# Performance work log

Measured on AMD Instinct MI355X. Metric: run time of the kernel, lower is better.

The kernel has to match this reference:

```python
import jax, jax.numpy as jnp
import numpy as np

N = 100000
E = 1600000
BN_EPS = 1e-3  # Keras BatchNormalization default epsilon


def setup_inputs() -> dict:
    key = jax.random.key(0)
    ks = jax.random.split(key, 24)
    inp = {
        'x': jax.random.normal(ks[0], (N, 128), jnp.float32),
        'edge_src': jax.random.randint(ks[1], (E,), 0, N, jnp.int32),
        'edge_dst': jnp.sort(jax.random.randint(ks[2], (E,), 0, N, jnp.int32)),
        'edge_w': jax.random.uniform(ks[3], (E,), jnp.float32),
        'bn1_gamma': jnp.ones((128,), jnp.float32),
        'bn1_beta': jnp.zeros((128,), jnp.float32),
        'bn1_mean': jax.random.normal(ks[4], (128,), jnp.float32),
        'bn1_var': jax.random.uniform(ks[5], (128,), jnp.float32),
        'gat_w': jax.random.normal(ks[6], (128, 128), jnp.float32) * 0.09,
        'gat_a_self': jax.random.normal(ks[7], (128,), jnp.float32) * 0.09,
        'gat_a_nbr': jax.random.normal(ks[8], (128,), jnp.float32) * 0.09,
        'gat_b': jnp.zeros((128,), jnp.float32),
        'bn2_gamma': jnp.ones((128,), jnp.float32),
        'bn2_beta': jnp.zeros((128,), jnp.float32),
        'bn2_mean': jax.random.normal(ks[9], (128,), jnp.float32),
        'bn2_var': jax.random.uniform(ks[10], (128,), jnp.float32),
        'gcn2_w': jax.random.normal(ks[11], (128, 64), jnp.float32) * 0.09,
        'gcn2_b': jnp.zeros((64,), jnp.float32),
        'bn3_gamma': jnp.ones((64,), jnp.float32),
        'bn3_beta': jnp.zeros((64,), jnp.float32),
        'bn3_mean': jax.random.normal(ks[12], (64,), jnp.float32),
        'bn3_var': jax.random.uniform(ks[13], (64,), jnp.float32),
        'gcn3_w': jax.random.normal(ks[14], (64, 32), jnp.float32) * 0.12,
        'gcn3_b': jnp.zeros((32,), jnp.float32),
        'zm_w': jax.random.normal(ks[15], (32, 64), jnp.float32) * 0.18,
        'zm_b': jnp.zeros((64,), jnp.float32),
        'zv_w': jax.random.normal(ks[16], (32, 64), jnp.float32) * 0.18,
        'zv_b': jnp.zeros((64,), jnp.float32),
        'eps': jax.random.normal(ks[17], (N, 64), jnp.float32),
    }
    return inp


def _bn(x, gamma, beta, mean, var):
    # Keras BatchNormalization, inference mode (moving statistics).
    return gamma * (x - mean) * jax.lax.rsqrt(var + BN_EPS) + beta


def _gat(x, edge_src, edge_dst, w, a_self, a_nbr, b, n):
    h = x @ w                                   # [N, C]
    att_i = h @ a_self                          # [N] target score
    att_j = h @ a_nbr                           # [N] source score
    e = jax.nn.leaky_relu(att_i[edge_dst] + att_j[edge_src], 0.2)  # [E]
    m = jax.ops.segment_max(e, edge_dst, num_segments=n)
    p = jnp.exp(e - m[edge_dst])
    s = jax.ops.segment_sum(p, edge_dst, num_segments=n)
    alpha = p / s[edge_dst]                     # segment softmax over in-edges
    out = jax.ops.segment_sum(alpha[:, None] * h[edge_src], edge_dst, num_segments=n)
    return jax.nn.relu(out + b)


def _gcn(x, edge_src, edge_dst, edge_w, w, b, n):
    h = x @ w                                   # [N, C]
    out = jax.ops.segment_sum(edge_w[:, None] * h[edge_src], edge_dst, num_segments=n)
    return jax.nn.relu(out + b)


def reference(x, edge_src, edge_dst, edge_w,
              bn1_gamma, bn1_beta, bn1_mean, bn1_var,
              gat_w, gat_a_self, gat_a_nbr, gat_b,
              bn2_gamma, bn2_beta, bn2_mean, bn2_var,
              gcn2_w, gcn2_b,
              bn3_gamma, bn3_beta, bn3_mean, bn3_var,
              gcn3_w, gcn3_b,
              zm_w, zm_b, zv_w, zv_b, eps):
    n = x.shape[0]
    h = _bn(x, bn1_gamma, bn1_beta, bn1_mean, bn1_var)
    h = _gat(h, edge_src, edge_dst, gat_w, gat_a_self, gat_a_nbr, gat_b, n)
    # dropout layers are identity at inference
    h = _bn(h, bn2_gamma, bn2_beta, bn2_mean, bn2_var)
    h = _gcn(h, edge_src, edge_dst, edge_w, gcn2_w, gcn2_b, n)
    h = _bn(h, bn3_gamma, bn3_beta, bn3_mean, bn3_var)
    h = _gcn(h, edge_src, edge_dst, edge_w, gcn3_w, gcn3_b, n)
    # Flatten on [N, F] is identity
    z_mean = jax.nn.sigmoid(h @ zm_w + zm_b)
    z_log_var = h @ zv_w + zv_b
    z = z_mean + jnp.exp(0.5 * z_log_var) * eps
    return (z_mean, z_log_var, z)
```

## Files before the change

kernel.cpp:

```cpp
#include <hip/hip_runtime.h>
#include <math.h>


#define BN_EPS 1e-3f

typedef __attribute__((ext_vector_type(8))) short bf16x8;
typedef __attribute__((ext_vector_type(4))) float f32x4;
typedef __attribute__((ext_vector_type(2))) float f32x2;

__device__ __forceinline__ f32x2 pkfma(f32x2 a, f32x2 b, f32x2 c) {
  f32x2 d;
  asm("v_pk_fma_f32 %0, %1, %2, %3" : "=v"(d) : "v"(a), "v"(b), "v"(c));
  return d;
}

__device__ __forceinline__ unsigned bf2(float lo, float hi) {
  unsigned ul = __float_as_uint(lo), uh = __float_as_uint(hi);
  ul = (ul + 0x7FFFu + ((ul >> 16) & 1u)) >> 16;
  uh = (uh + 0x7FFFu + ((uh >> 16) & 1u)) >> 16;
  return ul | (uh << 16);
}
__device__ __forceinline__ unsigned short bf1(float x) {
  unsigned u = __float_as_uint(x);
  return (unsigned short)((u + 0x7FFFu + ((u >> 16) & 1u)) >> 16);
}
__device__ __forceinline__ f32x2 ub2(unsigned u) {
  f32x2 r;
  r.x = __uint_as_float(u << 16);
  r.y = __uint_as_float(u & 0xFFFF0000u);
  return r;
}

__global__ __launch_bounds__(256) void prep_rowptr_kernel(
    const float* __restrict__ bn1g, const float* __restrict__ bn1b,
    const float* __restrict__ bn1m, const float* __restrict__ bn1v,
    const float* __restrict__ gatw,
    const float* __restrict__ bn2g, const float* __restrict__ bn2b,
    const float* __restrict__ bn2m, const float* __restrict__ bn2v,
    const float* __restrict__ gcn2w,
    const float* __restrict__ bn3g, const float* __restrict__ bn3b,
    const float* __restrict__ bn3m, const float* __restrict__ bn3v,
    const float* __restrict__ gcn3w,
    unsigned short* __restrict__ Wt1b, float* __restrict__ bW1,
    unsigned short* __restrict__ Wt2b, float* __restrict__ bW2,
    unsigned short* __restrict__ Wt3b, float* __restrict__ bW3,
    const int* __restrict__ dst, int* __restrict__ rp, int n, int e) {
  const int t = threadIdx.x;
  if (blockIdx.x != 0) {
    int i = (blockIdx.x - 1) * 256 + t;
    if (i > n) return;
    int lo = 0, hi = e;
    while (lo < hi) {
      int mid = (lo + hi) >> 1;
      if (dst[mid] < i) lo = mid + 1; else hi = mid;
    }
    rp[i] = lo;
    return;
  }
  __shared__ float a1[128], b1[128], a2[128], b2[128], a3[64], b3[64];
  if (t < 128) {
    float a = bn1g[t] * (1.0f / sqrtf(bn1v[t] + BN_EPS));
    a1[t] = a; b1[t] = bn1b[t] - bn1m[t] * a;
    float c = bn2g[t] * (1.0f / sqrtf(bn2v[t] + BN_EPS));
    a2[t] = c; b2[t] = bn2b[t] - bn2m[t] * c;
    if (t < 64) {
      float d = bn3g[t] * (1.0f / sqrtf(bn3v[t] + BN_EPS));
      a3[t] = d; b3[t] = bn3b[t] - bn3m[t] * d;
    }
  }
  __syncthreads();
  for (int idx = t; idx < 128 * 128; idx += 256) {
    int c = idx >> 7, k = idx & 127;
    Wt1b[idx] = bf1(a1[k] * gatw[k * 128 + c]);
  }
  for (int idx = t; idx < 64 * 128; idx += 256) {
    int c = idx >> 7, k = idx & 127;
    Wt2b[idx] = bf1(a2[k] * gcn2w[k * 64 + c]);
  }
  for (int idx = t; idx < 32 * 64; idx += 256) {
    int c = idx >> 6, k = idx & 63;
    Wt3b[idx] = bf1(a3[k] * gcn3w[k * 32 + c]);
  }
  if (t < 128) { float s = 0.f; for (int k = 0; k < 128; k++) s += b1[k] * gatw[k * 128 + t]; bW1[t] = s; }
  if (t < 64)  { float s = 0.f; for (int k = 0; k < 128; k++) s += b2[k] * gcn2w[k * 64 + t]; bW2[t] = s; }
  if (t < 32)  { float s = 0.f; for (int k = 0; k < 64; k++)  s += b3[k] * gcn3w[k * 32 + t]; bW3[t] = s; }
}

template <int K, int C, bool DO_ATT, bool IN_BF16>
__global__ __launch_bounds__(256) void gemm_mfma(
    const void* __restrict__ in, const unsigned short* __restrict__ Wtb,
    const float* __restrict__ bW, unsigned short* __restrict__ outb, int n,
    const float* __restrict__ aself, const float* __restrict__ anbr,
    float* __restrict__ atti, float* __restrict__ attj) {
  constexpr int KCH = K / 32;
  constexpr int MB = C / 16;
  const int wid = (blockIdx.x << 2) + (threadIdx.x >> 6);
  const int lane = threadIdx.x & 63;
  const int node0 = wid * 16;
  if (node0 >= n) return;
  const int ln = lane & 15;
  const int kg = lane >> 4;
  const int nd = node0 + ln;
  const int ndc = (nd < n) ? nd : (n - 1);
  bf16x8 bfr[KCH];
  if constexpr (IN_BF16) {
    const bf16x8* __restrict__ inr =
        (const bf16x8*)((const unsigned short*)in + (size_t)ndc * K);
#pragma unroll
    for (int kc = 0; kc < KCH; kc++) bfr[kc] = inr[kc * 4 + kg];
  } else {
    const float4* __restrict__ inr =
        (const float4*)((const float*)in + (size_t)ndc * K);
#pragma unroll
    for (int kc = 0; kc < KCH; kc++) {
      float4 u0 = inr[kc * 8 + kg * 2];
      float4 u1 = inr[kc * 8 + kg * 2 + 1];
      union { uint4 u; bf16x8 v; } pk;
      pk.u.x = bf2(u0.x, u0.y); pk.u.y = bf2(u0.z, u0.w);
      pk.u.z = bf2(u1.x, u1.y); pk.u.w = bf2(u1.z, u1.w);
      bfr[kc] = pk.v;
    }
  }
  float sa = 0.f, sj = 0.f;
#pragma unroll
  for (int m = 0; m < MB; m++) {
    f32x4 acc = {0.f, 0.f, 0.f, 0.f};
#pragma unroll
    for (int kc = 0; kc < KCH; kc++) {
      bf16x8 af = *(const bf16x8*)&Wtb[(size_t)(m * 16 + ln) * K + kc * 32 + kg * 8];
      acc = __builtin_amdgcn_mfma_f32_16x16x32_bf16(af, bfr[kc], acc, 0, 0, 0);
    }
    const int c0 = m * 16 + kg * 4;
    float4 bv = *(const float4*)&bW[c0];
    float o0 = acc[0] + bv.x, o1 = acc[1] + bv.y;
    float o2 = acc[2] + bv.z, o3 = acc[3] + bv.w;
    if (nd < n) {
      uint2 p; p.x = bf2(o0, o1); p.y = bf2(o2, o3);
      *(uint2*)&outb[(size_t)nd * C + c0] = p;
    }
    if constexpr (DO_ATT) {
      float4 as = *(const float4*)&aself[c0];
      float4 an = *(const float4*)&anbr[c0];
      sa += o0 * as.x + o1 * as.y + o2 * as.z + o3 * as.w;
      sj += o0 * an.x + o1 * an.y + o2 * an.z + o3 * an.w;
    }
  }
  if constexpr (DO_ATT) {
    sa += __shfl_xor(sa, 16); sa += __shfl_xor(sa, 32);
    sj += __shfl_xor(sj, 16); sj += __shfl_xor(sj, 32);
    if (kg == 0 && nd < n) { atti[nd] = sa; attj[nd] = sj; }
  }
}

__global__ __launch_bounds__(256) void gat_kernel(
    const unsigned short* __restrict__ h1b, const float* __restrict__ att_i,
    const float* __restrict__ att_j, const int* __restrict__ src,
    const int* __restrict__ rp, const float* __restrict__ bias,
    unsigned short* __restrict__ outb, int n) {
  const int node = (blockIdx.x * 256 + threadIdx.x) >> 5;
  const int sl = threadIdx.x & 31;
  const int gbase = threadIdx.x & 32;
  if (node >= n) return;
  const int start = rp[node];
  const int deg = rp[node + 1] - start;
  if (deg == 0) {
    float4 b = ((const float4*)bias)[sl];
    uint2 p;
    p.x = bf2(fmaxf(b.x, 0.f), fmaxf(b.y, 0.f));
    p.y = bf2(fmaxf(b.z, 0.f), fmaxf(b.w, 0.f));
    ((uint2*)outb)[(unsigned)node * 32 + sl] = p;
    return;
  }
  const uint2* __restrict__ h2v = (const uint2*)h1b;
  const float ai = att_i[node];
  f32x2 av[8];
#pragma unroll
  for (int k = 0; k < 8; k++) av[k] = {0.f, 0.f};
  float ss = 0.f, m_run = -INFINITY;
  for (int chunk = 0; chunk < deg; chunk += 32) {
    const int cnt = min(32, deg - chunk);
    int sv = 0; float v = -INFINITY;
    if (sl < cnt) {
      sv = src[start + chunk + sl];
      float a = ai + att_j[sv];
      v = (a >= 0.f) ? a : 0.2f * a;
    }
    float m = v;
#pragma unroll
    for (int off = 16; off; off >>= 1) m = fmaxf(m, __shfl_xor(m, off));
    const float m_new = fmaxf(m_run, m);
    if (chunk) {
      const float scale = __expf(m_run - m_new);
#pragma unroll
      for (int k = 0; k < 8; k++) { av[k].x *= scale; av[k].y *= scale; }
      ss *= scale;
    }
    const float p = (sl < cnt) ? __expf(v - m_new) : 0.f;
    float ps = p;
#pragma unroll
    for (int off = 16; off; off >>= 1) ps += __shfl_xor(ps, off);
    ss += ps;
    m_run = m_new;
    for (int j2 = 0; j2 < cnt; j2 += 8) {
      float pk[8]; int sk[8];
#pragma unroll
      for (int k = 0; k < 8; k++) {
        int j = gbase + j2 + k;
        pk[k] = __shfl(p, j);
        sk[k] = __shfl(sv, j);
      }
      uint2 hk[8];
#pragma unroll
      for (int k = 0; k < 8; k++) hk[k] = h2v[(unsigned)sk[k] * 32 + sl];
#pragma unroll
      for (int k = 0; k < 8; k++) {
        f32x2 pd = {pk[k], pk[k]};
        av[(k & 3) * 2]     = pkfma(ub2(hk[k].x), pd, av[(k & 3) * 2]);
        av[(k & 3) * 2 + 1] = pkfma(ub2(hk[k].y), pd, av[(k & 3) * 2 + 1]);
      }
    }
  }
  f32x2 s0, s1;
  s0.x = av[0].x + av[2].x + av[4].x + av[6].x;
  s0.y = av[0].y + av[2].y + av[4].y + av[6].y;
  s1.x = av[1].x + av[3].x + av[5].x + av[7].x;
  s1.y = av[1].y + av[3].y + av[5].y + av[7].y;
  const float inv = 1.0f / ss;
  float4 b = ((const float4*)bias)[sl];
  float o0 = fmaxf(fmaf(s0.x, inv, b.x), 0.f);
  float o1 = fmaxf(fmaf(s0.y, inv, b.y), 0.f);
  float o2 = fmaxf(fmaf(s1.x, inv, b.z), 0.f);
  float o3 = fmaxf(fmaf(s1.y, inv, b.w), 0.f);
  uint2 p; p.x = bf2(o0, o1); p.y = bf2(o2, o3);
  ((uint2*)outb)[(unsigned)node * 32 + sl] = p;
}

template <int C, int NCH>
__global__ __launch_bounds__(256) void gcn_agg_kernel(
    const unsigned short* __restrict__ hb, const int* __restrict__ src,
    const float* __restrict__ ew, const int* __restrict__ rp,
    const float* __restrict__ bias, unsigned short* __restrict__ outb, int n) {
  constexpr int CG = C / 4;
  constexpr int EGN = 64 / CG;
  const int node = (blockIdx.x * 256 + threadIdx.x) >> 6;
  const int lane = threadIdx.x & 63;
  if (node >= n) return;
  const int cg = lane % CG;
  const int eg = lane / CG;
  const int start = rp[node];
  const int deg = rp[node + 1] - start;
  const uint2* __restrict__ h2v = (const uint2*)hb;
  f32x2 av[8];
#pragma unroll
  for (int k = 0; k < 8; k++) av[k] = {0.f, 0.f};
  for (int chunk = 0; chunk < deg; chunk += 64) {
    const int cnt = min(64, deg - chunk);
    int sv = 0; float wv = 0.f;
    if (lane < cnt) {
      sv = src[start + chunk + lane];
      wv = ew[start + chunk + lane];
    }
    for (int j2 = 0; j2 < cnt; j2 += NCH * EGN) {
      float wk[NCH]; int sk[NCH];
#pragma unroll
      for (int k = 0; k < NCH; k++) {
        int j = j2 + k * EGN + eg;
        wk[k] = __shfl(wv, j);
        sk[k] = __shfl(sv, j);
      }
      uint2 hk[NCH];
#pragma unroll
      for (int k = 0; k < NCH; k++) hk[k] = h2v[(unsigned)sk[k] * CG + cg];
#pragma unroll
      for (int k = 0; k < NCH; k++) {
        f32x2 wd = {wk[k], wk[k]};
        av[(k & 3) * 2]     = pkfma(ub2(hk[k].x), wd, av[(k & 3) * 2]);
        av[(k & 3) * 2 + 1] = pkfma(ub2(hk[k].y), wd, av[(k & 3) * 2 + 1]);
      }
    }
  }
  float a0 = av[0].x + av[2].x + av[4].x + av[6].x;
  float a1 = av[0].y + av[2].y + av[4].y + av[6].y;
  float a2 = av[1].x + av[3].x + av[5].x + av[7].x;
  float a3 = av[1].y + av[3].y + av[5].y + av[7].y;
#pragma unroll
  for (int off = CG; off < 64; off <<= 1) {
    a0 += __shfl_xor(a0, off); a1 += __shfl_xor(a1, off);
    a2 += __shfl_xor(a2, off); a3 += __shfl_xor(a3, off);
  }
  if (eg == 0) {
    float4 b = ((const float4*)bias)[cg];
    float o0 = fmaxf(a0 + b.x, 0.f);
    float o1 = fmaxf(a1 + b.y, 0.f);
    float o2 = fmaxf(a2 + b.z, 0.f);
    float o3 = fmaxf(a3 + b.w, 0.f);
    uint2 p; p.x = bf2(o0, o1); p.y = bf2(o2, o3);
    ((uint2*)outb)[(unsigned)node * CG + cg] = p;
  }
}

__global__ __launch_bounds__(256) void final_kernel(
    const unsigned short* __restrict__ g3b, const float* __restrict__ zmw,
    const float* __restrict__ zmb, const float* __restrict__ zvw,
    const float* __restrict__ zvb, const float* __restrict__ eps,
    float* __restrict__ out, int n) {
  __shared__ float wm[32 * 64];
  __shared__ float wv[32 * 64];
  __shared__ float xs[4 * 32];
  for (int idx = threadIdx.x; idx < 2048; idx += 256) {
    wm[idx] = zmw[idx];
    wv[idx] = zvw[idx];
  }
  const float bm = zmb[threadIdx.x & 63];
  const float bv = zvb[threadIdx.x & 63];
  const size_t n64 = (size_t)n * 64;
  for (int pass = 0; pass < 16; pass++) {
    const int nb = blockIdx.x * 64 + pass * 4;
    __syncthreads();
    if (threadIdx.x < 128) {
      size_t idx = (size_t)nb * 32 + threadIdx.x;
      float vv = 0.f;
      if (idx < (size_t)n * 32)
        vv = __uint_as_float((unsigned)g3b[idx] << 16);
      xs[threadIdx.x] = vv;
    }
    __syncthreads();
    const int node = nb + (threadIdx.x >> 6);
    if (node >= n) continue;
    const int c = threadIdx.x & 63;
    const float* x = &xs[(threadIdx.x >> 6) * 32];
    float am = 0.f, avv = 0.f;
#pragma unroll
    for (int k = 0; k < 32; k++) {
      float xv = x[k];
      am = fmaf(xv, wm[k * 64 + c], am);
      avv = fmaf(xv, wv[k * 64 + c], avv);
    }
    am += bm;
    avv += bv;
    float zm = 1.f / (1.f + __expf(-am));
    float ex = __expf(fminf(0.5f * avv, 85.0f));
    float z = fmaf(ex, eps[(size_t)node * 64 + c], zm);
    size_t o = (size_t)node * 64 + c;
    out[o] = zm;
    out[n64 + o] = avv;
    out[2 * n64 + o] = z;
  }
}

extern "C" void kernel_launch(void* const* d_in, const int* in_sizes, int n_in,
                              void* d_out, int out_size, void* d_ws, size_t ws_size,
                              hipStream_t stream) {
  const float* x     = (const float*)d_in[0];
  const int*   esrc  = (const int*)d_in[1];
  const int*   edst  = (const int*)d_in[2];
  const float* ew    = (const float*)d_in[3];
  const float* bn1g  = (const float*)d_in[4];
  const float* bn1b  = (const float*)d_in[5];
  const float* bn1m  = (const float*)d_in[6];
  const float* bn1v  = (const float*)d_in[7];
  const float* gatw  = (const float*)d_in[8];
  const float* aself = (const float*)d_in[9];
  const float* anbr  = (const float*)d_in[10];
  const float* gatb  = (const float*)d_in[11];
  const float* bn2g  = (const float*)d_in[12];
  const float* bn2b  = (const float*)d_in[13];
  const float* bn2m  = (const float*)d_in[14];
  const float* bn2v  = (const float*)d_in[15];
  const float* gcn2w = (const float*)d_in[16];
  const float* gcn2b = (const float*)d_in[17];
  const float* bn3g  = (const float*)d_in[18];
  const float* bn3b  = (const float*)d_in[19];
  const float* bn3m  = (const float*)d_in[20];
  const float* bn3v  = (const float*)d_in[21];
  const float* gcn3w = (const float*)d_in[22];
  const float* gcn3b = (const float*)d_in[23];
  const float* zmw   = (const float*)d_in[24];
  const float* zmb   = (const float*)d_in[25];
  const float* zvw   = (const float*)d_in[26];
  const float* zvb   = (const float*)d_in[27];
  const float* eps   = (const float*)d_in[28];
  float* out = (float*)d_out;

  const int n = in_sizes[0] / 128;
  const int E = in_sizes[1];

  char* base = (char*)d_ws;
  size_t off = 0;
  auto alloc = [&](size_t bytes) -> char* {
    char* p = base + off;
    off += (bytes + 255) & ~(size_t)255;
    return p;
  };
  int*   rp   = (int*)alloc((size_t)(n + 1) * 4);
  unsigned short* Wt1b = (unsigned short*)alloc(128 * 128 * 2);
  float* bW1  = (float*)alloc(128 * 4);
  unsigned short* Wt2b = (unsigned short*)alloc(64 * 128 * 2);
  float* bW2  = (float*)alloc(64 * 4);
  unsigned short* Wt3b = (unsigned short*)alloc(32 * 64 * 2);
  float* bW3  = (float*)alloc(32 * 4);
  float* atti = (float*)alloc((size_t)n * 4);
  float* attj = (float*)alloc((size_t)n * 4);
  unsigned short* h1b = (unsigned short*)alloc((size_t)n * 128 * 2);
  unsigned short* g1b = (unsigned short*)alloc((size_t)n * 128 * 2);
  unsigned short* h2b = (unsigned short*)alloc((size_t)n * 64 * 2);
  unsigned short* g2b = h1b;
  unsigned short* h3b = g1b;
  unsigned short* g3b = h2b;

  const int rpb = (n + 1 + 255) / 256;
  prep_rowptr_kernel<<<rpb + 1, 256, 0, stream>>>(
      bn1g, bn1b, bn1m, bn1v, gatw, bn2g, bn2b, bn2m, bn2v, gcn2w,
      bn3g, bn3b, bn3m, bn3v, gcn3w,
      Wt1b, bW1, Wt2b, bW2, Wt3b, bW3, edst, rp, n, E);

  const int gw = (n + 15) / 16;
  const int gb = (gw + 3) / 4;

  gemm_mfma<128, 128, true, false><<<gb, 256, 0, stream>>>(
      x, Wt1b, bW1, h1b, n, aself, anbr, atti, attj);
  gat_kernel<<<(n + 7) / 8, 256, 0, stream>>>(
      h1b, atti, attj, esrc, rp, gatb, g1b, n);

  gemm_mfma<128, 64, false, true><<<gb, 256, 0, stream>>>(
      g1b, Wt2b, bW2, h2b, n, nullptr, nullptr, nullptr, nullptr);
  gcn_agg_kernel<64, 8><<<(n + 3) / 4, 256, 0, stream>>>(
      h2b, esrc, ew, rp, gcn2b, g2b, n);

  gemm_mfma<64, 32, false, true><<<gb, 256, 0, stream>>>(
      g2b, Wt3b, bW3, h3b, n, nullptr, nullptr, nullptr, nullptr);
  gcn_agg_kernel<32, 4><<<(n + 3) / 4, 256, 0, stream>>>(
      h3b, esrc, ew, rp, gcn3b, g3b, n);

  final_kernel<<<(n + 63) / 64, 256, 0, stream>>>(
      g3b, zmw, zmb, zvw, zvb, eps, out, n);
}
```

Baseline: 438.5 us.

## Map GCN aggregation to lane subgroups per node instead of whole wavefronts

The GCN aggregation kernel now gives each destination node a subgroup of C/4 lanes (16 or 8) instead of a full 64-lane wavefront. Several nodes therefore share one wavefront, and each subgroup walks its own edges serially. This drops the cross-lane xor-reduction and the wasted lanes that came from spreading low-degree nodes across a whole wave. The cost is more divergence between subgroups whose degrees differ, and longer serial edge loops for high-degree nodes. Grid sizes are adjusted to match, and the C=32 case now unrolls 8 edges at a time.

New measurement: 413.2 us. 5.8% less time.

```diff
diff --git a/kernel.cpp b/kernel.cpp
--- a/kernel.cpp
+++ b/kernel.cpp
@@ -236,41 +236,40 @@
 }
 
 template <int C, int NCH>
-__global__ __launch_bounds__(256) void gcn_agg_kernel(
+__global__ __launch_bounds__(256) void gcn_agg_sg_kernel(
     const unsigned short* __restrict__ hb, const int* __restrict__ src,
     const float* __restrict__ ew, const int* __restrict__ rp,
     const float* __restrict__ bias, unsigned short* __restrict__ outb, int n) {
-  constexpr int CG = C / 4;
-  constexpr int EGN = 64 / CG;
-  const int node = (blockIdx.x * 256 + threadIdx.x) >> 6;
-  const int lane = threadIdx.x & 63;
+  constexpr int SGL = C / 4;
+  const int lane6 = threadIdx.x & 63;
+  const int sl = lane6 & (SGL - 1);
+  const int gbase = lane6 & ~(SGL - 1);
+  const int node = (int)(((unsigned)(blockIdx.x * 256 + threadIdx.x)) / SGL);
   if (node >= n) return;
-  const int cg = lane % CG;
-  const int eg = lane / CG;
   const int start = rp[node];
   const int deg = rp[node + 1] - start;
   const uint2* __restrict__ h2v = (const uint2*)hb;
   f32x2 av[8];
 #pragma unroll
   for (int k = 0; k < 8; k++) av[k] = {0.f, 0.f};
-  for (int chunk = 0; chunk < deg; chunk += 64) {
-    const int cnt = min(64, deg - chunk);
+  for (int chunk = 0; chunk < deg; chunk += SGL) {
+    const int cnt = min(SGL, deg - chunk);
     int sv = 0; float wv = 0.f;
-    if (lane < cnt) {
-      sv = src[start + chunk + lane];
-      wv = ew[start + chunk + lane];
-    }
-    for (int j2 = 0; j2 < cnt; j2 += NCH * EGN) {
+    if (sl < cnt) {
+      sv = src[start + chunk + sl];
+      wv = ew[start + chunk + sl];
+    }
+    for (int j2 = 0; j2 < cnt; j2 += NCH) {
       float wk[NCH]; int sk[NCH];
 #pragma unroll
       for (int k = 0; k < NCH; k++) {
-        int j = j2 + k * EGN + eg;
+        int j = gbase + j2 + k;
         wk[k] = __shfl(wv, j);
         sk[k] = __shfl(sv, j);
       }
       uint2 hk[NCH];
 #pragma unroll
-      for (int k = 0; k < NCH; k++) hk[k] = h2v[(unsigned)sk[k] * CG + cg];
+      for (int k = 0; k < NCH; k++) hk[k] = h2v[(unsigned)sk[k] * SGL + sl];
 #pragma unroll
       for (int k = 0; k < NCH; k++) {
         f32x2 wd = {wk[k], wk[k]};
@@ -283,20 +282,13 @@
   float a1 = av[0].y + av[2].y + av[4].y + av[6].y;
   float a2 = av[1].x + av[3].x + av[5].x + av[7].x;
   float a3 = av[1].y + av[3].y + av[5].y + av[7].y;
-#pragma unroll
-  for (int off = CG; off < 64; off <<= 1) {
-    a0 += __shfl_xor(a0, off); a1 += __shfl_xor(a1, off);
-    a2 += __shfl_xor(a2, off); a3 += __shfl_xor(a3, off);
-  }
-  if (eg == 0) {
-    float4 b = ((const float4*)bias)[cg];
-    float o0 = fmaxf(a0 + b.x, 0.f);
-    float o1 = fmaxf(a1 + b.y, 0.f);
-    float o2 = fmaxf(a2 + b.z, 0.f);
-    float o3 = fmaxf(a3 + b.w, 0.f);
-    uint2 p; p.x = bf2(o0, o1); p.y = bf2(o2, o3);
-    ((uint2*)outb)[(unsigned)node * CG + cg] = p;
-  }
+  float4 b = ((const float4*)bias)[sl];
+  float o0 = fmaxf(a0 + b.x, 0.f);
+  float o1 = fmaxf(a1 + b.y, 0.f);
+  float o2 = fmaxf(a2 + b.z, 0.f);
+  float o3 = fmaxf(a3 + b.w, 0.f);
+  uint2 p; p.x = bf2(o0, o1); p.y = bf2(o2, o3);
+  ((uint2*)outb)[(unsigned)node * SGL + sl] = p;
 }
 
 __global__ __launch_bounds__(256) void final_kernel(
@@ -424,12 +416,12 @@
 
   gemm_mfma<128, 64, false, true><<<gb, 256, 0, stream>>>(
       g1b, Wt2b, bW2, h2b, n, nullptr, nullptr, nullptr, nullptr);
-  gcn_agg_kernel<64, 8><<<(n + 3) / 4, 256, 0, stream>>>(
+  gcn_agg_sg_kernel<64, 8><<<(n + 15) / 16, 256, 0, stream>>>(
       h2b, esrc, ew, rp, gcn2b, g2b, n);
 
   gemm_mfma<64, 32, false, true><<<gb, 256, 0, stream>>>(
       g2b, Wt3b, bW3, h3b, n, nullptr, nullptr, nullptr, nullptr);
-  gcn_agg_kernel<32, 4><<<(n + 3) / 4, 256, 0, stream>>>(
+  gcn_agg_sg_kernel<32, 8><<<(n + 31) / 32, 256, 0, stream>>>(
       h3b, esrc, ew, rp, gcn3b, g3b, n);
 
   final_kernel<<<(n + 63) / 64, 256, 0, stream>>>(
```
